# Performance work log

Hardware: AMD Instinct MI355X
Metric: run time of the kernel (lower is better)

## Reference

```python
import jax, jax.numpy as jnp
import numpy as np

N_NODES = 50000
N_EDGES = 800000
DIM_IN = 128
DIM_OUT = 64
HEADS = 4
NEG_SLOPE = 0.2


def setup_inputs() -> dict:
    key = jax.random.key(0)
    k_x, k_e, k_w, k_a = jax.random.split(key, 4)
    x = jax.random.normal(k_x, (N_NODES, DIM_IN), dtype=jnp.float32)
    edge_index = jax.random.randint(k_e, (2, N_EDGES), 0, N_NODES, dtype=jnp.int32)
    # Stacked per-head params: W (Linear(dim_in, dim_out, bias=False)) and
    # a (Linear(2*dim_out, 1, bias=False)) for each of HEADS heads.
    W = jax.random.normal(k_w, (HEADS, DIM_IN, DIM_OUT), dtype=jnp.float32) * (1.0 / np.sqrt(DIM_IN))
    a = jax.random.normal(k_a, (HEADS, 2 * DIM_OUT), dtype=jnp.float32) * (1.0 / np.sqrt(2 * DIM_OUT))
    return {"x": x, "edge_index": edge_index, "W": W, "a": a}


def _gat_forward(x, W, a, edge_index):
    src = edge_index[0]  # segment for softmax / scatter target
    dst = edge_index[1]  # node whose features are gathered (x_j)
    # h: [N, H, D]
    h = jnp.einsum('nd,hdo->nho', x, W)
    a_i = a[:, :DIM_OUT]   # [H, D] applied to x_i
    a_j = a[:, DIM_OUT:]   # [H, D] applied to x_j
    # per-node attention logit halves: [N, H]
    s_i = jnp.einsum('nhd,hd->nh', h, a_i)
    s_j = jnp.einsum('nhd,hd->nh', h, a_j)
    e = jax.nn.leaky_relu(s_i[src] + s_j[dst], NEG_SLOPE)  # [E, H]
    # segment softmax over edges grouped by src node
    m = jax.ops.segment_max(e, src, num_segments=N_NODES)  # [N, H]
    ex = jnp.exp(e - m[src])
    denom = jax.ops.segment_sum(ex, src, num_segments=N_NODES)  # [N, H]
    att = ex / denom[src]  # [E, H]
    # weighted scatter-sum of gathered features: [N, H, D]
    msgs = att[:, :, None] * h[dst]
    h_prime = jax.ops.segment_sum(msgs, src, num_segments=N_NODES)
    # concat=False -> mean over heads
    return jnp.mean(h_prime, axis=1)  # [N, D]


def reference(x, edge_index, W, a):
    return _gat_forward(x, W, a, edge_index)
```

## Files before the change

### kernel.cpp

```cpp
#include <hip/hip_runtime.h>
#include <hip/hip_bf16.h>

#define N_NODES 50000
#define N_EDGES 800000
#define DIM_IN  128
#define DIM_OUT 64
#define HEADS   4
#define NEG_SLOPE 0.2f
#define NPB 32
#define GEMM_BLOCKS ((N_NODES + NPB - 1) / NPB)
#define N_PAD (GEMM_BLOCKS * NPB)
#define PAD 64
#define CHUNKS 128
#define EPC (N_EDGES / CHUNKS)
#define CPITCH 50048
#define HWORDS (CPITCH / 2)
#define SCAN_BLOCKS ((HWORDS + 255) / 256)
#define FAT_GRID (SCAN_BLOCKS + GEMM_BLOCKS)
#define XROW 136
#define LTROW 260

typedef __attribute__((ext_vector_type(8))) short short8;
typedef __attribute__((ext_vector_type(4))) short short4v;
typedef __attribute__((ext_vector_type(4))) float f32x4;

__device__ __forceinline__ unsigned int f2bf(float f) {
    unsigned int u = __float_as_uint(f);
    return (u + 0x7FFFu + ((u >> 16) & 1u)) >> 16;
}
__device__ __forceinline__ float bf2f(unsigned int b) {
    return __uint_as_float(b << 16);
}

__global__ __launch_bounds__(512) void prep_count_kernel(
    const float* __restrict__ W, unsigned short* __restrict__ Wph,
    unsigned short* __restrict__ Wpl, const int* __restrict__ ei,
    unsigned short* __restrict__ cnt)
{
    __shared__ unsigned int hist[HWORDS];
    const int b = blockIdx.x;
    const int t = threadIdx.x;
    if (b < 8) {
        const int i = b * 512 + t;
        const int lane = i & 63, nt = (i >> 6) & 3, kc = (i >> 8) & 3, h = (i >> 10) & 3;
        const int col = lane & 15, quad = lane >> 4;
        unsigned short hv[8], lv[8];
#pragma unroll
        for (int j = 0; j < 8; ++j) {
            const int k = kc * 32 + quad * 8 + j;
            const int n = nt * 16 + col;
            const float f = W[h * (DIM_IN * DIM_OUT) + k * DIM_OUT + n];
            const unsigned int hb = f2bf(f);
            hv[j] = (unsigned short)hb;
            lv[j] = (unsigned short)f2bf(f - bf2f(hb));
        }
        *(short8*)(Wph + (size_t)i * 8) = *(short8*)hv;
        *(short8*)(Wpl + (size_t)i * 8) = *(short8*)lv;
        return;
    }
    const int c = b - 8;
    for (int i = t; i < HWORDS; i += 512) hist[i] = 0;
    __syncthreads();
    const int* srcp = ei + c * EPC;
    for (int e = t; e < EPC; e += 512) {
        const int s = srcp[e];
        atomicAdd(&hist[s >> 1], 1u << ((s & 1) * 16));
    }
    __syncthreads();
    unsigned int* rowp = (unsigned int*)(cnt + (size_t)c * CPITCH);
    for (int i = t; i < HWORDS; i += 512) rowp[i] = hist[i];
}

__global__ __launch_bounds__(256) void fat_kernel(
    const float* __restrict__ x, const unsigned short* __restrict__ Wph,
    const unsigned short* __restrict__ Wpl, const float* __restrict__ a,
    unsigned short* __restrict__ h2, float* __restrict__ s_i, float* __restrict__ s_j,
    unsigned short* __restrict__ cnt, int* __restrict__ cursor)
{
    __shared__ __align__(16) unsigned char smem[2 * NPB * XROW * 2];
    const int b = blockIdx.x;
    const int t = threadIdx.x;

    if (b < SCAN_BLOCKS) {
        const int i = b * 256 + t;
        if (i < HWORDS) {
            unsigned int* p = (unsigned int*)cnt + i;
            unsigned int runlo = 0, runhi = 0;
#pragma unroll
            for (int c0 = 0; c0 < CHUNKS; c0 += 16) {
                unsigned int v[16];
#pragma unroll
                for (int q = 0; q < 16; ++q) v[q] = p[(size_t)(c0 + q) * HWORDS];
#pragma unroll
                for (int q = 0; q < 16; ++q) {
                    p[(size_t)(c0 + q) * HWORDS] = runlo | (runhi << 16);
                    runlo += v[q] & 0xFFFFu;
                    runhi += v[q] >> 16;
                }
            }
            const int n0 = i * 2;
            if (n0 < N_NODES) cursor[n0] = (int)runlo;
            if (n0 + 1 < N_NODES) cursor[n0 + 1] = (int)runhi;
        }
        return;
    }

    short* xh = (short*)smem;
    short* xl = xh + NPB * XROW;
    const int nb = (b - SCAN_BLOCKS) * NPB;

    {
        const float4* xg = (const float4*)x;
        const int base = nb * (DIM_IN / 4);
        const int limit = N_NODES * (DIM_IN / 4);
#pragma unroll
        for (int r = 0; r < 4; ++r) {
            const int idx = t + 256 * r;
            const int gi = base + idx;
            float4 v = {0.f, 0.f, 0.f, 0.f};
            if (gi < limit) v = xg[gi];
            const int node = idx >> 5;
            const int dg = (idx & 31) * 4;
            unsigned short hs[4], ls[4];
            const float fv[4] = {v.x, v.y, v.z, v.w};
#pragma unroll
            for (int c = 0; c < 4; ++c) {
                const unsigned int hb = f2bf(fv[c]);
                hs[c] = (unsigned short)hb;
                ls[c] = (unsigned short)f2bf(fv[c] - bf2f(hb));
            }
            *(short4v*)(xh + node * XROW + dg) = *(short4v*)hs;
            *(short4v*)(xl + node * XROW + dg) = *(short4v*)ls;
        }
    }
    __syncthreads();

    const int w = t >> 6;
    const int lane = t & 63;
    const int col = lane & 15, quad = lane >> 4;

    f32x4 acc[2][4];
#pragma unroll
    for (int mt = 0; mt < 2; ++mt)
#pragma unroll
        for (int nt = 0; nt < 4; ++nt) acc[mt][nt] = (f32x4){0.f, 0.f, 0.f, 0.f};

    const short8* Bh = (const short8*)Wph;
    const short8* Bl = (const short8*)Wpl;
#pragma unroll
    for (int kc = 0; kc < 4; ++kc) {
        const short8 ah0 = *(const short8*)(xh + (0 * 16 + col) * XROW + kc * 32 + quad * 8);
        const short8 al0 = *(const short8*)(xl + (0 * 16 + col) * XROW + kc * 32 + quad * 8);
        const short8 ah1 = *(const short8*)(xh + (1 * 16 + col) * XROW + kc * 32 + quad * 8);
        const short8 al1 = *(const short8*)(xl + (1 * 16 + col) * XROW + kc * 32 + quad * 8);
#pragma unroll
        for (int nt = 0; nt < 4; ++nt) {
            const int fi = ((w * 4 + kc) * 4 + nt) * 64 + lane;
            const short8 bh = Bh[fi];
            const short8 bl = Bl[fi];
            acc[0][nt] = __builtin_amdgcn_mfma_f32_16x16x32_bf16(ah0, bh, acc[0][nt], 0, 0, 0);
            acc[0][nt] = __builtin_amdgcn_mfma_f32_16x16x32_bf16(al0, bh, acc[0][nt], 0, 0, 0);
            acc[0][nt] = __builtin_amdgcn_mfma_f32_16x16x32_bf16(ah0, bl, acc[0][nt], 0, 0, 0);
            acc[1][nt] = __builtin_amdgcn_mfma_f32_16x16x32_bf16(ah1, bh, acc[1][nt], 0, 0, 0);
            acc[1][nt] = __builtin_amdgcn_mfma_f32_16x16x32_bf16(al1, bh, acc[1][nt], 0, 0, 0);
            acc[1][nt] = __builtin_amdgcn_mfma_f32_16x16x32_bf16(ah1, bl, acc[1][nt], 0, 0, 0);
        }
    }

    float aiv[4], ajv[4];
#pragma unroll
    for (int nt = 0; nt < 4; ++nt) {
        aiv[nt] = a[w * (2 * DIM_OUT) + nt * 16 + col];
        ajv[nt] = a[w * (2 * DIM_OUT) + DIM_OUT + nt * 16 + col];
    }
#pragma unroll
    for (int mt = 0; mt < 2; ++mt) {
#pragma unroll
        for (int r = 0; r < 4; ++r) {
            float pi = 0.f, pj = 0.f;
#pragma unroll
            for (int nt = 0; nt < 4; ++nt) {
                pi = fmaf(acc[mt][nt][r], aiv[nt], pi);
                pj = fmaf(acc[mt][nt][r], ajv[nt], pj);
            }
#pragma unroll
            for (int off = 8; off > 0; off >>= 1) {
                pi += __shfl_down(pi, off, 16);
                pj += __shfl_down(pj, off, 16);
            }
            if (col == 0) {
                const int n = nb + mt * 16 + quad * 4 + r;
                s_i[n * HEADS + w] = pi;
                s_j[n * HEADS + w] = pj;
            }
        }
    }
    __syncthreads();

    short* lt = (short*)smem;
#pragma unroll
    for (int mt = 0; mt < 2; ++mt)
#pragma unroll
        for (int nt = 0; nt < 4; ++nt)
#pragma unroll
            for (int r = 0; r < 4; ++r)
                lt[(mt * 16 + quad * 4 + r) * LTROW + (nt * 16 + col) * 4 + w] =
                    (short)f2bf(acc[mt][nt][r]);
    __syncthreads();

    uint2* hg = (uint2*)(h2 + (size_t)nb * (DIM_OUT * HEADS));
#pragma unroll
    for (int r = 0; r < 8; ++r) {
        const int idx = t + 256 * r;
        const int node = idx >> 6;
        const int wo = idx & 63;
        hg[idx] = *(const uint2*)(lt + node * LTROW + wo * 4);
    }
}

__global__ __launch_bounds__(512) void scatter_kernel(
    const int* __restrict__ ei, const unsigned short* __restrict__ cnt,
    unsigned short* __restrict__ sdst)
{
    __shared__ unsigned int cur[HWORDS];
    const int c = blockIdx.x;
    const int t = threadIdx.x;
    const unsigned int* rowp = (const unsigned int*)(cnt + (size_t)c * CPITCH);
    for (int i = t; i < HWORDS; i += 512) cur[i] = rowp[i];
    __syncthreads();
    const int* srcp = ei + c * EPC;
    const int* dstp = ei + N_EDGES + c * EPC;
    for (int e = t; e < EPC; e += 512) {
        const int s = srcp[e];
        const int d = dstp[e];
        const unsigned int sh = (unsigned int)(s & 1) * 16u;
        const unsigned int old = atomicAdd(&cur[s >> 1], 1u << sh);
        const unsigned int slot = (old >> sh) & 0xFFFFu;
        if (slot < PAD) sdst[s * PAD + slot] = (unsigned short)d;
    }
}

__global__ __launch_bounds__(256) void fused_kernel(
    const int* __restrict__ cursor, const unsigned short* __restrict__ sdst,
    const float* __restrict__ s_i, const float* __restrict__ s_j,
    const unsigned short* __restrict__ h2, float* __restrict__ out)
{
    __shared__ float4 att_s[4][64];
    __shared__ int    dst_s[4][64];
    const int wid = (blockIdx.x * 256 + threadIdx.x) >> 6;
    const int w = (threadIdx.x >> 6) & 3;
    const int lane = threadIdx.x & 63;
    if (wid >= N_NODES) return;
    const int n = wid;
    const int d = min(cursor[n], PAD);
    const int start = n * PAD;

    float acc = 0.f;
    if (d > 0) {
        const float4 si = *(const float4*)(s_i + n * HEADS);
        float4 m4 = {-INFINITY, -INFINITY, -INFINITY, -INFINITY};
        float4 cz = {-INFINITY, -INFINITY, -INFINITY, -INFINITY};
        int cdst = 0;
        if (lane < d) {
            cdst = (int)sdst[start + lane];
            const float4 sj = *(const float4*)(s_j + cdst * HEADS);
            float z0 = si.x + sj.x, z1 = si.y + sj.y, z2 = si.z + sj.z, z3 = si.w + sj.w;
            cz.x = z0 >= 0.f ? z0 : NEG_SLOPE * z0;
            cz.y = z1 >= 0.f ? z1 : NEG_SLOPE * z1;
            cz.z = z2 >= 0.f ? z2 : NEG_SLOPE * z2;
            cz.w = z3 >= 0.f ? z3 : NEG_SLOPE * z3;
            m4 = cz;
        }
#pragma unroll
        for (int off = 32; off > 0; off >>= 1) {
            m4.x = fmaxf(m4.x, __shfl_xor(m4.x, off, 64));
            m4.y = fmaxf(m4.y, __shfl_xor(m4.y, off, 64));
            m4.z = fmaxf(m4.z, __shfl_xor(m4.z, off, 64));
            m4.w = fmaxf(m4.w, __shfl_xor(m4.w, off, 64));
        }
        float4 ex = {0.f, 0.f, 0.f, 0.f};
        if (lane < d) {
            ex.x = __expf(cz.x - m4.x);
            ex.y = __expf(cz.y - m4.y);
            ex.z = __expf(cz.z - m4.z);
            ex.w = __expf(cz.w - m4.w);
        }
        float4 sm = ex;
#pragma unroll
        for (int off = 32; off > 0; off >>= 1) {
            sm.x += __shfl_xor(sm.x, off, 64);
            sm.y += __shfl_xor(sm.y, off, 64);
            sm.z += __shfl_xor(sm.z, off, 64);
            sm.w += __shfl_xor(sm.w, off, 64);
        }
        if (lane < d) {
            att_s[w][lane] = make_float4(ex.x / sm.x, ex.y / sm.y, ex.z / sm.z, ex.w / sm.w);
            dst_s[w][lane] = cdst;
        }

        const unsigned short* hbase = h2 + lane * HEADS;
        int e = 0;
        for (; e + 8 <= d; e += 8) {
            uint2 hv[8];
            float4 at[8];
#pragma unroll
            for (int q = 0; q < 8; ++q) {
                const int dd = dst_s[w][e + q];
                at[q] = att_s[w][e + q];
                hv[q] = *(const uint2*)(hbase + (size_t)dd * (DIM_OUT * HEADS));
            }
#pragma unroll
            for (int q = 0; q < 8; ++q) {
                acc += at[q].x * bf2f(hv[q].x & 0xFFFFu) + at[q].y * bf2f(hv[q].x >> 16)
                     + at[q].z * bf2f(hv[q].y & 0xFFFFu) + at[q].w * bf2f(hv[q].y >> 16);
            }
        }
        for (; e + 4 <= d; e += 4) {
            uint2 hv[4];
            float4 at[4];
#pragma unroll
            for (int q = 0; q < 4; ++q) {
                const int dd = dst_s[w][e + q];
                at[q] = att_s[w][e + q];
                hv[q] = *(const uint2*)(hbase + (size_t)dd * (DIM_OUT * HEADS));
            }
#pragma unroll
            for (int q = 0; q < 4; ++q) {
                acc += at[q].x * bf2f(hv[q].x & 0xFFFFu) + at[q].y * bf2f(hv[q].x >> 16)
                     + at[q].z * bf2f(hv[q].y & 0xFFFFu) + at[q].w * bf2f(hv[q].y >> 16);
            }
        }
        for (; e < d; ++e) {
            const int dd = dst_s[w][e];
            const float4 a4 = att_s[w][e];
            const uint2 hv = *(const uint2*)(hbase + (size_t)dd * (DIM_OUT * HEADS));
            acc += a4.x * bf2f(hv.x & 0xFFFFu) + a4.y * bf2f(hv.x >> 16)
                 + a4.z * bf2f(hv.y & 0xFFFFu) + a4.w * bf2f(hv.y >> 16);
        }
    }
    out[n * DIM_OUT + lane] = 0.25f * acc;
}

extern "C" void kernel_launch(void* const* d_in, const int* in_sizes, int n_in,
                              void* d_out, int out_size, void* d_ws, size_t ws_size,
                              hipStream_t stream) {
    const float* x  = (const float*)d_in[0];
    const int*   ei = (const int*)d_in[1];
    const float* W  = (const float*)d_in[2];
    const float* a  = (const float*)d_in[3];
    float* out = (float*)d_out;

    char* ws = (char*)d_ws;
    size_t off = 0;
    auto alloc = [&](size_t bytes) { void* p = ws + off; off = (off + bytes + 511) & ~size_t(511); return p; };
    unsigned short* h2  = (unsigned short*)alloc(sizeof(unsigned short) * N_PAD * DIM_OUT * HEADS);
    float* s_i    = (float*)alloc(sizeof(float) * N_PAD * HEADS);
    float* s_j    = (float*)alloc(sizeof(float) * N_PAD * HEADS);
    int*   cursor = (int*)alloc(sizeof(int) * N_NODES);
    unsigned short* sdst = (unsigned short*)alloc(sizeof(unsigned short) * N_NODES * PAD);
    unsigned short* cnt  = (unsigned short*)alloc(sizeof(unsigned short) * CHUNKS * CPITCH);
    unsigned short* Wph  = (unsigned short*)alloc(sizeof(unsigned short) * HEADS * DIM_IN * DIM_OUT);
    unsigned short* Wpl  = (unsigned short*)alloc(sizeof(unsigned short) * HEADS * DIM_IN * DIM_OUT);

    prep_count_kernel<<<8 + CHUNKS, 512, 0, stream>>>(W, Wph, Wpl, ei, cnt);

    fat_kernel<<<FAT_GRID, 256, 0, stream>>>(x, Wph, Wpl, a, h2, s_i, s_j, cnt, cursor);

    scatter_kernel<<<CHUNKS, 512, 0, stream>>>(ei, cnt, sdst);

    const int fb = (N_NODES * 64 + 255) / 256;
    fused_kernel<<<fb, 256, 0, stream>>>(cursor, sdst, s_i, s_j, h2, out);
}
```

Before: 180.1 us.

## Double-buffer neighbor feature gathers and widen count/scatter blocks to 1024 threads

The aggregation kernel now issues the first batch of neighbor feature loads before the softmax reductions and alternates two register buffers, so the gather for the next batch overlaps the FMA work on the current one. Softmax normalisation moves to a single division at the end, and the accumulation is split into four per-head FMA chains. Padding lanes are zeroed so that every batch is a full group of eight and no tail loops are needed. The histogram and scatter kernels use 1024-thread blocks, which adds more warps per chunk for latency hiding at the cost of higher register pressure per block.

```diff
diff --git a/kernel.cpp b/kernel.cpp
--- a/kernel.cpp
+++ b/kernel.cpp
@@ -32,7 +32,7 @@
     return __uint_as_float(b << 16);
 }
 
-__global__ __launch_bounds__(512) void prep_count_kernel(
+__global__ __launch_bounds__(1024) void prep_count_kernel(
     const float* __restrict__ W, unsigned short* __restrict__ Wph,
     unsigned short* __restrict__ Wpl, const int* __restrict__ ei,
     unsigned short* __restrict__ cnt)
@@ -40,8 +40,8 @@
     __shared__ unsigned int hist[HWORDS];
     const int b = blockIdx.x;
     const int t = threadIdx.x;
-    if (b < 8) {
-        const int i = b * 512 + t;
+    if (b < 4) {
+        const int i = b * 1024 + t;
         const int lane = i & 63, nt = (i >> 6) & 3, kc = (i >> 8) & 3, h = (i >> 10) & 3;
         const int col = lane & 15, quad = lane >> 4;
         unsigned short hv[8], lv[8];
@@ -58,17 +58,17 @@
         *(short8*)(Wpl + (size_t)i * 8) = *(short8*)lv;
         return;
     }
-    const int c = b - 8;
-    for (int i = t; i < HWORDS; i += 512) hist[i] = 0;
+    const int c = b - 4;
+    for (int i = t; i < HWORDS; i += 1024) hist[i] = 0;
     __syncthreads();
     const int* srcp = ei + c * EPC;
-    for (int e = t; e < EPC; e += 512) {
+    for (int e = t; e < EPC; e += 1024) {
         const int s = srcp[e];
         atomicAdd(&hist[s >> 1], 1u << ((s & 1) * 16));
     }
     __syncthreads();
     unsigned int* rowp = (unsigned int*)(cnt + (size_t)c * CPITCH);
-    for (int i = t; i < HWORDS; i += 512) rowp[i] = hist[i];
+    for (int i = t; i < HWORDS; i += 1024) rowp[i] = hist[i];
 }
 
 __global__ __launch_bounds__(256) void fat_kernel(
@@ -218,7 +218,7 @@
     }
 }
 
-__global__ __launch_bounds__(512) void scatter_kernel(
+__global__ __launch_bounds__(1024) void scatter_kernel(
     const int* __restrict__ ei, const unsigned short* __restrict__ cnt,
     unsigned short* __restrict__ sdst)
 {
@@ -226,11 +226,11 @@
     const int c = blockIdx.x;
     const int t = threadIdx.x;
     const unsigned int* rowp = (const unsigned int*)(cnt + (size_t)c * CPITCH);
-    for (int i = t; i < HWORDS; i += 512) cur[i] = rowp[i];
+    for (int i = t; i < HWORDS; i += 1024) cur[i] = rowp[i];
     __syncthreads();
     const int* srcp = ei + c * EPC;
     const int* dstp = ei + N_EDGES + c * EPC;
-    for (int e = t; e < EPC; e += 512) {
+    for (int e = t; e < EPC; e += 1024) {
         const int s = srcp[e];
         const int d = dstp[e];
         const unsigned int sh = (unsigned int)(s & 1) * 16u;
@@ -255,7 +255,6 @@
     const int d = min(cursor[n], PAD);
     const int start = n * PAD;
 
-    float acc = 0.f;
     if (d > 0) {
         const float4 si = *(const float4*)(s_i + n * HEADS);
         float4 m4 = {-INFINITY, -INFINITY, -INFINITY, -INFINITY};
@@ -271,6 +270,29 @@
             cz.w = z3 >= 0.f ? z3 : NEG_SLOPE * z3;
             m4 = cz;
         }
+        dst_s[w][lane] = (lane < d) ? cdst : 0;
+
+        const unsigned short* hbase = h2 + lane * HEADS;
+        const int nb8 = (d + 7) >> 3;
+        uint2 hvA[8], hvB[8];
+
+        auto PF_A = [&](int bb) {
+#pragma unroll
+            for (int q = 0; q < 8; ++q) {
+                const int dd = dst_s[w][bb * 8 + q];
+                hvA[q] = *(const uint2*)(hbase + (size_t)dd * (DIM_OUT * HEADS));
+            }
+        };
+        auto PF_B = [&](int bb) {
+#pragma unroll
+            for (int q = 0; q < 8; ++q) {
+                const int dd = dst_s[w][bb * 8 + q];
+                hvB[q] = *(const uint2*)(hbase + (size_t)dd * (DIM_OUT * HEADS));
+            }
+        };
+
+        PF_A(0);
+
 #pragma unroll
         for (int off = 32; off > 0; off >>= 1) {
             m4.x = fmaxf(m4.x, __shfl_xor(m4.x, off, 64));
@@ -293,52 +315,46 @@
             sm.z += __shfl_xor(sm.z, off, 64);
             sm.w += __shfl_xor(sm.w, off, 64);
         }
-        if (lane < d) {
-            att_s[w][lane] = make_float4(ex.x / sm.x, ex.y / sm.y, ex.z / sm.z, ex.w / sm.w);
-            dst_s[w][lane] = cdst;
-        }
-
-        const unsigned short* hbase = h2 + lane * HEADS;
-        int e = 0;
-        for (; e + 8 <= d; e += 8) {
-            uint2 hv[8];
-            float4 at[8];
+        att_s[w][lane] = (lane < d) ? ex : make_float4(0.f, 0.f, 0.f, 0.f);
+
+        float a0 = 0.f, a1 = 0.f, a2 = 0.f, a3 = 0.f;
+        auto CS_A = [&](int bb) {
 #pragma unroll
             for (int q = 0; q < 8; ++q) {
-                const int dd = dst_s[w][e + q];
-                at[q] = att_s[w][e + q];
-                hv[q] = *(const uint2*)(hbase + (size_t)dd * (DIM_OUT * HEADS));
-            }
+                const float4 at = att_s[w][bb * 8 + q];
+                const uint2 v = hvA[q];
+                a0 = fmaf(at.x, __uint_as_float(v.x << 16), a0);
+                a1 = fmaf(at.y, __uint_as_float(v.x & 0xFFFF0000u), a1);
+                a2 = fmaf(at.z, __uint_as_float(v.y << 16), a2);
+                a3 = fmaf(at.w, __uint_as_float(v.y & 0xFFFF0000u), a3);
+            }
+        };
+        auto CS_B = [&](int bb) {
 #pragma unroll
             for (int q = 0; q < 8; ++q) {
-                acc += at[q].x * bf2f(hv[q].x & 0xFFFFu) + at[q].y * bf2f(hv[q].x >> 16)
-                     + at[q].z * bf2f(hv[q].y & 0xFFFFu) + at[q].w * bf2f(hv[q].y >> 16);
-            }
-        }
-        for (; e + 4 <= d; e += 4) {
-            uint2 hv[4];
-            float4 at[4];
-#pragma unroll
-            for (int q = 0; q < 4; ++q) {
-                const int dd = dst_s[w][e + q];
-                at[q] = att_s[w][e + q];
-                hv[q] = *(const uint2*)(hbase + (size_t)dd * (DIM_OUT * HEADS));
-            }
-#pragma unroll
-            for (int q = 0; q < 4; ++q) {
-                acc += at[q].x * bf2f(hv[q].x & 0xFFFFu) + at[q].y * bf2f(hv[q].x >> 16)
-                     + at[q].z * bf2f(hv[q].y & 0xFFFFu) + at[q].w * bf2f(hv[q].y >> 16);
-            }
-        }
-        for (; e < d; ++e) {
-            const int dd = dst_s[w][e];
-            const float4 a4 = att_s[w][e];
-            const uint2 hv = *(const uint2*)(hbase + (size_t)dd * (DIM_OUT * HEADS));
-            acc += a4.x * bf2f(hv.x & 0xFFFFu) + a4.y * bf2f(hv.x >> 16)
-                 + a4.z * bf2f(hv.y & 0xFFFFu) + a4.w * bf2f(hv.y >> 16);
-        }
-    }
-    out[n * DIM_OUT + lane] = 0.25f * acc;
+                const float4 at = att_s[w][bb * 8 + q];
+                const uint2 v = hvB[q];
+                a0 = fmaf(at.x, __uint_as_float(v.x << 16), a0);
+                a1 = fmaf(at.y, __uint_as_float(v.x & 0xFFFF0000u), a1);
+                a2 = fmaf(at.z, __uint_as_float(v.y << 16), a2);
+                a3 = fmaf(at.w, __uint_as_float(v.y & 0xFFFF0000u), a3);
+            }
+        };
+
+        int bb = 0;
+        while (true) {
+            if (bb + 1 < nb8) PF_B(bb + 1);
+            CS_A(bb);
+            ++bb; if (bb >= nb8) break;
+            if (bb + 1 < nb8) PF_A(bb + 1);
+            CS_B(bb);
+            ++bb; if (bb >= nb8) break;
+        }
+
+        out[n * DIM_OUT + lane] = 0.25f * (a0 / sm.x + a1 / sm.y + a2 / sm.z + a3 / sm.w);
+    } else {
+        out[n * DIM_OUT + lane] = 0.f;
+    }
 }
 
 extern "C" void kernel_launch(void* const* d_in, const int* in_sizes, int n_in,
@@ -362,11 +378,11 @@
     unsigned short* Wph  = (unsigned short*)alloc(sizeof(unsigned short) * HEADS * DIM_IN * DIM_OUT);
     unsigned short* Wpl  = (unsigned short*)alloc(sizeof(unsigned short) * HEADS * DIM_IN * DIM_OUT);
 
-    prep_count_kernel<<<8 + CHUNKS, 512, 0, stream>>>(W, Wph, Wpl, ei, cnt);
+    prep_count_kernel<<<4 + CHUNKS, 1024, 0, stream>>>(W, Wph, Wpl, ei, cnt);
 
     fat_kernel<<<FAT_GRID, 256, 0, stream>>>(x, Wph, Wpl, a, h2, s_i, s_j, cnt, cursor);
 
-    scatter_kernel<<<CHUNKS, 512, 0, stream>>>(ei, cnt, sdst);
+    scatter_kernel<<<CHUNKS, 1024, 0, stream>>>(ei, cnt, sdst);
 
     const int fb = (N_NODES * 64 + 255) / 256;
     fused_kernel<<<fb, 256, 0, stream>>>(cursor, sdst, s_i, s_j, h2, out);
```

Measured after the change: 177.3 us. No clear change (-1.5%).

## Replace per-node chunk histograms with two-level range bucketing for CSR build

Applied to the files above, without the earlier changes.

The CSR build no longer keeps a full 50k-entry per-chunk count table. Edges are first bucketed into 128 source-node ranges using a tiny histogram and a single-block scan. A new per-range kernel then assigns slots with shared-memory atomics and writes the padded adjacency and per-node degree. This drops the large 128x50k count scan and its memory traffic. In exchange it adds a kernel launch, an intermediate edge buffer, and a per-range pass that only 128 blocks run, which limits parallelism.

```diff
diff --git a/kernel.cpp b/kernel.cpp
--- a/kernel.cpp
+++ b/kernel.cpp
@@ -13,10 +13,9 @@
 #define PAD 64
 #define CHUNKS 128
 #define EPC (N_EDGES / CHUNKS)
-#define CPITCH 50048
-#define HWORDS (CPITCH / 2)
-#define SCAN_BLOCKS ((HWORDS + 255) / 256)
-#define FAT_GRID (SCAN_BLOCKS + GEMM_BLOCKS)
+#define RANGES 128
+#define RSPAN 391
+#define HTOT (RANGES * CHUNKS)
 #define XROW 136
 #define LTROW 260
 
@@ -32,16 +31,15 @@
     return __uint_as_float(b << 16);
 }
 
-__global__ __launch_bounds__(512) void prep_count_kernel(
+__global__ __launch_bounds__(256) void pack_hist_kernel(
     const float* __restrict__ W, unsigned short* __restrict__ Wph,
     unsigned short* __restrict__ Wpl, const int* __restrict__ ei,
-    unsigned short* __restrict__ cnt)
+    unsigned int* __restrict__ histT)
 {
-    __shared__ unsigned int hist[HWORDS];
     const int b = blockIdx.x;
     const int t = threadIdx.x;
-    if (b < 8) {
-        const int i = b * 512 + t;
+    if (b < 16) {
+        const int i = b * 256 + t;
         const int lane = i & 63, nt = (i >> 6) & 3, kc = (i >> 8) & 3, h = (i >> 10) & 3;
         const int col = lane & 15, quad = lane >> 4;
         unsigned short hv[8], lv[8];
@@ -58,56 +56,66 @@
         *(short8*)(Wpl + (size_t)i * 8) = *(short8*)lv;
         return;
     }
-    const int c = b - 8;
-    for (int i = t; i < HWORDS; i += 512) hist[i] = 0;
+    __shared__ unsigned int h4[4][RANGES];
+    const int c = b - 16;
+    const int w = t >> 6;
+    for (int i = t; i < 4 * RANGES; i += 256) ((unsigned int*)h4)[i] = 0u;
     __syncthreads();
     const int* srcp = ei + c * EPC;
-    for (int e = t; e < EPC; e += 512) {
+    for (int e = t; e < EPC; e += 256) {
         const int s = srcp[e];
-        atomicAdd(&hist[s >> 1], 1u << ((s & 1) * 16));
-    }
-    __syncthreads();
-    unsigned int* rowp = (unsigned int*)(cnt + (size_t)c * CPITCH);
-    for (int i = t; i < HWORDS; i += 512) rowp[i] = hist[i];
-}
-
-__global__ __launch_bounds__(256) void fat_kernel(
+        atomicAdd(&h4[w][s / RSPAN], 1u);
+    }
+    __syncthreads();
+    if (t < RANGES)
+        histT[t * CHUNKS + c] = h4[0][t] + h4[1][t] + h4[2][t] + h4[3][t];
+}
+
+__global__ __launch_bounds__(256) void scan_gemm_kernel(
     const float* __restrict__ x, const unsigned short* __restrict__ Wph,
     const unsigned short* __restrict__ Wpl, const float* __restrict__ a,
     unsigned short* __restrict__ h2, float* __restrict__ s_i, float* __restrict__ s_j,
-    unsigned short* __restrict__ cnt, int* __restrict__ cursor)
+    const unsigned int* __restrict__ histT, unsigned int* __restrict__ S)
 {
     __shared__ __align__(16) unsigned char smem[2 * NPB * XROW * 2];
     const int b = blockIdx.x;
     const int t = threadIdx.x;
 
-    if (b < SCAN_BLOCKS) {
-        const int i = b * 256 + t;
-        if (i < HWORDS) {
-            unsigned int* p = (unsigned int*)cnt + i;
-            unsigned int runlo = 0, runhi = 0;
-#pragma unroll
-            for (int c0 = 0; c0 < CHUNKS; c0 += 16) {
-                unsigned int v[16];
-#pragma unroll
-                for (int q = 0; q < 16; ++q) v[q] = p[(size_t)(c0 + q) * HWORDS];
-#pragma unroll
-                for (int q = 0; q < 16; ++q) {
-                    p[(size_t)(c0 + q) * HWORDS] = runlo | (runhi << 16);
-                    runlo += v[q] & 0xFFFFu;
-                    runhi += v[q] >> 16;
-                }
-            }
-            const int n0 = i * 2;
-            if (n0 < N_NODES) cursor[n0] = (int)runlo;
-            if (n0 + 1 < N_NODES) cursor[n0 + 1] = (int)runhi;
+    if (b == 0) {
+        unsigned int* part = (unsigned int*)smem;
+        const uint4* H4 = (const uint4*)histT;
+        unsigned int sum = 0;
+#pragma unroll
+        for (int q = 0; q < 16; ++q) {
+            const uint4 v = H4[t * 16 + q];
+            sum += v.x + v.y + v.z + v.w;
+        }
+        part[t] = sum;
+        __syncthreads();
+        for (int off = 1; off < 256; off <<= 1) {
+            const unsigned int v = (t >= off) ? part[t - off] : 0u;
+            __syncthreads();
+            part[t] += v;
+            __syncthreads();
+        }
+        unsigned int run = part[t] - sum;
+        uint4* S4 = (uint4*)S;
+#pragma unroll
+        for (int q = 0; q < 16; ++q) {
+            const uint4 v = H4[t * 16 + q];
+            uint4 o;
+            o.x = run; run += v.x;
+            o.y = run; run += v.y;
+            o.z = run; run += v.z;
+            o.w = run; run += v.w;
+            S4[t * 16 + q] = o;
         }
         return;
     }
 
     short* xh = (short*)smem;
     short* xl = xh + NPB * XROW;
-    const int nb = (b - SCAN_BLOCKS) * NPB;
+    const int nb = (b - 1) * NPB;
 
     {
         const float4* xg = (const float4*)x;
@@ -218,25 +226,48 @@
     }
 }
 
-__global__ __launch_bounds__(512) void scatter_kernel(
-    const int* __restrict__ ei, const unsigned short* __restrict__ cnt,
-    unsigned short* __restrict__ sdst)
+__global__ __launch_bounds__(512) void bucket_kernel(
+    const int* __restrict__ ei, const unsigned int* __restrict__ S,
+    unsigned int* __restrict__ ebuf)
 {
-    __shared__ unsigned int cur[HWORDS];
+    __shared__ unsigned int cur[RANGES];
     const int c = blockIdx.x;
     const int t = threadIdx.x;
-    const unsigned int* rowp = (const unsigned int*)(cnt + (size_t)c * CPITCH);
-    for (int i = t; i < HWORDS; i += 512) cur[i] = rowp[i];
+    if (t < RANGES) cur[t] = S[t * CHUNKS + c];
     __syncthreads();
     const int* srcp = ei + c * EPC;
     const int* dstp = ei + N_EDGES + c * EPC;
     for (int e = t; e < EPC; e += 512) {
         const int s = srcp[e];
         const int d = dstp[e];
-        const unsigned int sh = (unsigned int)(s & 1) * 16u;
-        const unsigned int old = atomicAdd(&cur[s >> 1], 1u << sh);
-        const unsigned int slot = (old >> sh) & 0xFFFFu;
-        if (slot < PAD) sdst[s * PAD + slot] = (unsigned short)d;
+        const int r = s / RSPAN;
+        const unsigned int pos = atomicAdd(&cur[r], 1u);
+        ebuf[pos] = ((unsigned int)(s - r * RSPAN) << 16) | (unsigned int)d;
+    }
+}
+
+__global__ __launch_bounds__(512) void csr_kernel(
+    const unsigned int* __restrict__ ebuf, const unsigned int* __restrict__ S,
+    unsigned short* __restrict__ sdst, int* __restrict__ cursor)
+{
+    __shared__ unsigned int cur[RSPAN];
+    const int r = blockIdx.x;
+    const int t = threadIdx.x;
+    const unsigned int j0 = S[r * CHUNKS];
+    const unsigned int j1 = (r + 1 < RANGES) ? S[(r + 1) * CHUNKS] : N_EDGES;
+    for (int i = t; i < RSPAN; i += 512) cur[i] = 0u;
+    __syncthreads();
+    for (unsigned int e = j0 + t; e < j1; e += 512) {
+        const unsigned int v = ebuf[e];
+        const unsigned int sl = v >> 16;
+        const unsigned int d = v & 0xFFFFu;
+        const unsigned int slot = atomicAdd(&cur[sl], 1u);
+        if (slot < PAD) sdst[(size_t)(r * RSPAN + sl) * PAD + slot] = (unsigned short)d;
+    }
+    __syncthreads();
+    for (int i = t; i < RSPAN; i += 512) {
+        const int n = r * RSPAN + i;
+        if (n < N_NODES) cursor[n] = (int)cur[i];
     }
 }
 
@@ -358,15 +389,19 @@
     float* s_j    = (float*)alloc(sizeof(float) * N_PAD * HEADS);
     int*   cursor = (int*)alloc(sizeof(int) * N_NODES);
     unsigned short* sdst = (unsigned short*)alloc(sizeof(unsigned short) * N_NODES * PAD);
-    unsigned short* cnt  = (unsigned short*)alloc(sizeof(unsigned short) * CHUNKS * CPITCH);
+    unsigned int* histT  = (unsigned int*)alloc(sizeof(unsigned int) * HTOT);
+    unsigned int* S      = (unsigned int*)alloc(sizeof(unsigned int) * HTOT);
+    unsigned int* ebuf   = (unsigned int*)alloc(sizeof(unsigned int) * N_EDGES);
     unsigned short* Wph  = (unsigned short*)alloc(sizeof(unsigned short) * HEADS * DIM_IN * DIM_OUT);
     unsigned short* Wpl  = (unsigned short*)alloc(sizeof(unsigned short) * HEADS * DIM_IN * DIM_OUT);
 
-    prep_count_kernel<<<8 + CHUNKS, 512, 0, stream>>>(W, Wph, Wpl, ei, cnt);
-
-    fat_kernel<<<FAT_GRID, 256, 0, stream>>>(x, Wph, Wpl, a, h2, s_i, s_j, cnt, cursor);
-
-    scatter_kernel<<<CHUNKS, 512, 0, stream>>>(ei, cnt, sdst);
+    pack_hist_kernel<<<16 + CHUNKS, 256, 0, stream>>>(W, Wph, Wpl, ei, histT);
+
+    scan_gemm_kernel<<<1 + GEMM_BLOCKS, 256, 0, stream>>>(x, Wph, Wpl, a, h2, s_i, s_j, histT, S);
+
+    bucket_kernel<<<CHUNKS, 512, 0, stream>>>(ei, S, ebuf);
+
+    csr_kernel<<<RANGES, 512, 0, stream>>>(ebuf, S, sdst, cursor);
 
     const int fb = (N_NODES * 64 + 255) / 256;
     fused_kernel<<<fb, 256, 0, stream>>>(cursor, sdst, s_i, s_j, h2, out);
```

Result: no change. 181.5 us (+0.8%).
